# Kernel optimization log

Measured on AMD Instinct MI355X. Metric: run time of the kernel, lower is better.

## Reference

```python
import math
import jax, jax.numpy as jnp
import numpy as np

B, T, C = 4, 2048, 1024
NH = 16
HD = C // NH  # 64

def setup_inputs() -> dict:
    key = jax.random.key(0)
    k1, k2, k3 = jax.random.split(key, 3)
    x = jax.random.normal(k1, (B, T, C), dtype=jnp.float32)
    # init scale ~ 1/sqrt(fan_in) to keep activations sane
    W_attn = jax.random.normal(k2, (C, 3 * C), dtype=jnp.float32) * (1.0 / math.sqrt(C))
    b_attn = jnp.zeros((3 * C,), dtype=jnp.float32)
    W_proj = jax.random.normal(k3, (C, C), dtype=jnp.float32) * (1.0 / math.sqrt(C))
    b_proj = jnp.zeros((C,), dtype=jnp.float32)
    return {"x": x, "W_attn": W_attn, "b_attn": b_attn, "W_proj": W_proj, "b_proj": b_proj}

def reference(x, W_attn, b_attn, W_proj, b_proj):
    b, t, c = x.shape
    qkv = x @ W_attn + b_attn                      # [B,T,3C]
    q, k, v = jnp.split(qkv, 3, axis=-1)           # each [B,T,C]
    # [B,T,C] -> [B,NH,T,HD]
    def heads(z):
        return z.reshape(b, t, NH, HD).transpose(0, 2, 1, 3)
    q, k, v = heads(q), heads(k), heads(v)
    scale = 1.0 / math.sqrt(HD)
    att = jnp.einsum('bhqd,bhkd->bhqk', q, k) * scale   # [B,NH,T,T]
    causal = jnp.tril(jnp.ones((t, t), dtype=bool))      # [T,T]
    att = jnp.where(causal[None, None, :, :], att, -jnp.inf)
    att = jax.nn.softmax(att, axis=-1)
    # dropout p=0.0 -> identity
    y = jnp.einsum('bhqk,bhkd->bhqd', att, v)            # [B,NH,T,HD]
    y = y.transpose(0, 2, 1, 3).reshape(b, t, c)         # [B,T,C]
    return y @ W_proj + b_proj
```

## Files before the change

kernel.cpp:

```cpp
#include <hip/hip_runtime.h>
#include <hip/hip_bf16.h>


typedef __bf16 bf16;
typedef __bf16 bf16x4 __attribute__((ext_vector_type(4)));
typedef __bf16 bf16x8 __attribute__((ext_vector_type(8)));
typedef float  f32x4  __attribute__((ext_vector_type(4)));

#define MFMA16(a, b, c) __builtin_amdgcn_mfma_f32_16x16x32_bf16((a), (b), (c), 0, 0, 0)

#define GLOAD16(g, l)                                                 \
    __builtin_amdgcn_global_load_lds(                                 \
        (const __attribute__((address_space(1))) void*)(g),           \
        (__attribute__((address_space(3))) void*)(l), 16, 0, 0)

static constexpr int Bsz = 4;
static constexpr int T   = 2048;
static constexpr int Cc  = 1024;
static constexpr int NH  = 16;
static constexpr int HD  = 64;
static constexpr int C3  = 3 * Cc;

__global__ void cvt_f32_bf16(const float* __restrict__ in, bf16* __restrict__ out) {
    size_t i = ((size_t)blockIdx.x * blockDim.x + threadIdx.x) * 8;
    f32x4 a0 = *(const f32x4*)(in + i);
    f32x4 a1 = *(const f32x4*)(in + i + 4);
    bf16x8 v;
#pragma unroll
    for (int e = 0; e < 4; ++e) { v[e] = (bf16)a0[e]; v[e + 4] = (bf16)a1[e]; }
    *(bf16x8*)(out + i) = v;
}

__global__ void transpose_f32_bf16(const float* __restrict__ in, bf16* __restrict__ out,
                                   int R, int Ccols) {
    __shared__ float tile[32][33];
    int bx = blockIdx.x * 32;
    int by = blockIdx.y * 32;
    int tx = threadIdx.x, ty = threadIdx.y;
#pragma unroll
    for (int i = 0; i < 32; i += 8)
        tile[ty + i][tx] = in[(size_t)(by + ty + i) * Ccols + bx + tx];
    __syncthreads();
#pragma unroll
    for (int i = 0; i < 32; i += 8)
        out[(size_t)(bx + ty + i) * R + by + tx] = (bf16)tile[tx][ty + i];
}

__global__ __launch_bounds__(256)
void gemm_qkv(const bf16* __restrict__ A, const bf16* __restrict__ Bt,
              const float* __restrict__ bias,
              bf16* __restrict__ qo, bf16* __restrict__ ko, bf16* __restrict__ vt,
              int M, int N, int K) {
    constexpr int BM = 128, BN = 128, BK = 64;
    __shared__ bf16 As[2][BM * BK];
    __shared__ bf16 Bs[2][BN * BK];

    const int tid  = threadIdx.x;
    const int wave = tid >> 6, lane = tid & 63;
    const int quad = lane >> 4, l16 = lane & 15;
    const int wm = wave & 1, wn = wave >> 1;
    const int m0 = blockIdx.x * BM, n0 = blockIdx.y * BN;

    f32x4 acc[4][4] = {};

    const int lrow = lane >> 3;
    const int lcol = (lane & 7) * 8;
    const bf16* Ab = A  + (size_t)(m0 + wave * 8 + lrow) * K + lcol;
    const bf16* Bb = Bt + (size_t)(n0 + wave * 8 + lrow) * K + lcol;
    const int wofs = wave * 512;

#pragma unroll
    for (int r = 0; r < 4; ++r) {
        GLOAD16(Ab + (size_t)r * 32 * K, As[0] + wofs + r * 2048);
        GLOAD16(Bb + (size_t)r * 32 * K, Bs[0] + wofs + r * 2048);
    }

    int cur = 0;
    for (int k0 = 0; k0 < K; k0 += BK) {
        __syncthreads();
        if (k0 + BK < K) {
#pragma unroll
            for (int r = 0; r < 4; ++r) {
                GLOAD16(Ab + (size_t)r * 32 * K + k0 + BK, As[cur ^ 1] + wofs + r * 2048);
                GLOAD16(Bb + (size_t)r * 32 * K + k0 + BK, Bs[cur ^ 1] + wofs + r * 2048);
            }
        }
        const bf16* Asc = As[cur];
        const bf16* Bsc = Bs[cur];
#pragma unroll
        for (int ks = 0; ks < 2; ++ks) {
            bf16x8 af[4], bfr[4];
#pragma unroll
            for (int i = 0; i < 4; ++i)
                af[i] = *(const bf16x8*)(&Asc[(wm * 64 + i * 16 + l16) * BK + ks * 32 + quad * 8]);
#pragma unroll
            for (int j = 0; j < 4; ++j)
                bfr[j] = *(const bf16x8*)(&Bsc[(wn * 64 + j * 16 + l16) * BK + ks * 32 + quad * 8]);
#pragma unroll
            for (int i = 0; i < 4; ++i)
#pragma unroll
                for (int j = 0; j < 4; ++j)
                    acc[i][j] = MFMA16(af[i], bfr[j], acc[i][j]);
        }
        cur ^= 1;
    }

    const int which = n0 >> 10;
    const int nc0 = n0 & 1023;
    if (which < 2) {
        bf16* dst = which ? ko : qo;
#pragma unroll
        for (int j = 0; j < 4; ++j) {
            int colg = n0 + wn * 64 + j * 16 + l16;
            int coll = nc0 + wn * 64 + j * 16 + l16;
            float bv = bias[colg];
#pragma unroll
            for (int i = 0; i < 4; ++i) {
                int rowb = m0 + wm * 64 + i * 16 + quad * 4;
#pragma unroll
                for (int r = 0; r < 4; ++r)
                    dst[(size_t)(rowb + r) * Cc + coll] = (bf16)(acc[i][j][r] + bv);
            }
        }
    } else {
#pragma unroll
        for (int j = 0; j < 4; ++j) {
            int colg = n0 + wn * 64 + j * 16 + l16;
            int coll = nc0 + wn * 64 + j * 16 + l16;
            int h = coll >> 6, d = coll & 63;
            float bv = bias[colg];
            bf16* vhead_d = vt + ((size_t)h * HD + d) * T;
#pragma unroll
            for (int i = 0; i < 4; ++i) {
                int rowb = m0 + wm * 64 + i * 16 + quad * 4;
                int b = rowb >> 11;
                int t = rowb & 2047;
                bf16x4 pk;
#pragma unroll
                for (int r = 0; r < 4; ++r) pk[r] = (bf16)(acc[i][j][r] + bv);
                *(bf16x4*)(vhead_d + (size_t)b * NH * HD * T + t) = pk;
            }
        }
    }
}

__global__ __launch_bounds__(256)
void gemm_bt(const bf16* __restrict__ A, const bf16* __restrict__ Bt,
             const float* __restrict__ bias, float* __restrict__ C,
             int M, int N, int K) {
    constexpr int BM = 128, BN = 128, BK = 64;
    __shared__ bf16 As[2][BM * BK];
    __shared__ bf16 Bs[2][BN * BK];

    const int tid  = threadIdx.x;
    const int wave = tid >> 6, lane = tid & 63;
    const int quad = lane >> 4, l16 = lane & 15;
    const int wm = wave & 1, wn = wave >> 1;
    const int m0 = blockIdx.x * BM, n0 = blockIdx.y * BN;

    f32x4 acc[4][4] = {};

    const int lrow = lane >> 3;
    const int lcol = (lane & 7) * 8;
    const bf16* Ab = A  + (size_t)(m0 + wave * 8 + lrow) * K + lcol;
    const bf16* Bb = Bt + (size_t)(n0 + wave * 8 + lrow) * K + lcol;
    const int wofs = wave * 512;

#pragma unroll
    for (int r = 0; r < 4; ++r) {
        GLOAD16(Ab + (size_t)r * 32 * K, As[0] + wofs + r * 2048);
        GLOAD16(Bb + (size_t)r * 32 * K, Bs[0] + wofs + r * 2048);
    }

    int cur = 0;
    for (int k0 = 0; k0 < K; k0 += BK) {
        __syncthreads();
        if (k0 + BK < K) {
#pragma unroll
            for (int r = 0; r < 4; ++r) {
                GLOAD16(Ab + (size_t)r * 32 * K + k0 + BK, As[cur ^ 1] + wofs + r * 2048);
                GLOAD16(Bb + (size_t)r * 32 * K + k0 + BK, Bs[cur ^ 1] + wofs + r * 2048);
            }
        }
        const bf16* Asc = As[cur];
        const bf16* Bsc = Bs[cur];
#pragma unroll
        for (int ks = 0; ks < 2; ++ks) {
            bf16x8 af[4], bfr[4];
#pragma unroll
            for (int i = 0; i < 4; ++i)
                af[i] = *(const bf16x8*)(&Asc[(wm * 64 + i * 16 + l16) * BK + ks * 32 + quad * 8]);
#pragma unroll
            for (int j = 0; j < 4; ++j)
                bfr[j] = *(const bf16x8*)(&Bsc[(wn * 64 + j * 16 + l16) * BK + ks * 32 + quad * 8]);
#pragma unroll
            for (int i = 0; i < 4; ++i)
#pragma unroll
                for (int j = 0; j < 4; ++j)
                    acc[i][j] = MFMA16(af[i], bfr[j], acc[i][j]);
        }
        cur ^= 1;
    }

#pragma unroll
    for (int j = 0; j < 4; ++j) {
        int col = n0 + wn * 64 + j * 16 + l16;
        float bv = bias[col];
#pragma unroll
        for (int i = 0; i < 4; ++i) {
            int rowb = m0 + wm * 64 + i * 16 + quad * 4;
#pragma unroll
            for (int r = 0; r < 4; ++r)
                C[(size_t)(rowb + r) * N + col] = acc[i][j][r] + bv;
        }
    }
}

__global__ __launch_bounds__(256, 4)
void attn_fused(const bf16* __restrict__ qb, const bf16* __restrict__ kb,
                const bf16* __restrict__ vtb, bf16* __restrict__ y) {
    constexpr int LKD = 72;
    constexpr int LVT = 40;
    constexpr int LPS = 40;
    constexpr int QT = T / 128;
    __shared__ bf16 Ks[2][32 * LKD];
    __shared__ bf16 Vt[2][64 * LVT];
    __shared__ bf16 Ps[4][32 * LPS];

    const int tid  = threadIdx.x;
    const int wave = tid >> 6, lane = tid & 63;
    const int quad = lane >> 4, l16 = lane & 15;
    const int bid = blockIdx.x;
    const int pr = bid >> 6;
    const int hb = bid & 63;
    const int b = hb >> 4, h = hb & 15;

    const bf16* qbase  = qb + (size_t)b * T * Cc + h * HD;
    const bf16* kbase  = kb + (size_t)b * T * Cc + h * HD;
    const bf16* vthead = vtb + (size_t)(b * NH + h) * HD * T;
    bf16* yrow = y + (size_t)b * T * Cc + h * HD;

    const int srK = tid >> 3, scK = (tid & 7) * 8;
    const int srV = tid >> 2, scV = (tid & 3) * 8;

    bf16x8 ones;
#pragma unroll
    for (int e = 0; e < 8; ++e) ones[e] = (bf16)1.0f;

#pragma unroll 1
    for (int seg = 0; seg < 2; ++seg) {
        const int qt = (seg == 0) ? (QT - 1 - pr) : pr;
        const int q0 = qt * 128;

        bf16x8 qf[2][2];
#pragma unroll
        for (int qn = 0; qn < 2; ++qn) {
            int qrow = q0 + wave * 32 + qn * 16 + l16;
#pragma unroll
            for (int dblk = 0; dblk < 2; ++dblk) {
                bf16x8 v = *(const bf16x8*)(qbase + (size_t)qrow * Cc + dblk * 32 + quad * 8);
#pragma unroll
                for (int e = 0; e < 8; ++e) v[e] = (bf16)((float)v[e] * 0.18033688f);
                qf[qn][dblk] = v;
            }
        }

        f32x4 o[2][4] = {};
        f32x4 osum[2] = {};

        const int w0 = q0 + wave * 32;
        const int nt = q0 / 32 + 4;

        bf16x8 kp = *(const bf16x8*)(kbase + (size_t)srK * Cc + scK);
        bf16x8 vp = *(const bf16x8*)(vthead + (size_t)srV * T + scV);
        __syncthreads();
        *(bf16x8*)(&Ks[0][srK * LKD + scK]) = kp;
        *(bf16x8*)(&Vt[0][srV * LVT + scV]) = vp;

        int cur = 0;
        for (int it = 0; it < nt; ++it) {
            const int kt = it * 32;
            __syncthreads();

            const bool more = (it + 1 < nt);
            if (more) {
                int ktn = kt + 32;
                kp = *(const bf16x8*)(kbase + (size_t)(ktn + srK) * Cc + scK);
                vp = *(const bf16x8*)(vthead + (size_t)srV * T + ktn + scV);
            }

            const bf16* ksc = Ks[cur];
            const bf16* vtc = Vt[cur];
            if (kt <= w0 + 31) {
                __builtin_amdgcn_s_setprio(1);
                f32x4 st[2][2] = {};
#pragma unroll
                for (int km = 0; km < 2; ++km) {
                    bf16x8 kf0 = *(const bf16x8*)(&ksc[(km * 16 + l16) * LKD + quad * 8]);
                    bf16x8 kf1 = *(const bf16x8*)(&ksc[(km * 16 + l16) * LKD + 32 + quad * 8]);
#pragma unroll
                    for (int qn = 0; qn < 2; ++qn) {
                        st[km][qn] = MFMA16(kf0, qf[qn][0], st[km][qn]);
                        st[km][qn] = MFMA16(kf1, qf[qn][1], st[km][qn]);
                    }
                }

                const bool needmask = (kt + 31 > w0);
#pragma unroll
                for (int km = 0; km < 2; ++km)
#pragma unroll
                    for (int qn = 0; qn < 2; ++qn) {
                        int qrel = w0 + qn * 16 + l16 - kt;
#pragma unroll
                        for (int r = 0; r < 4; ++r) {
                            float v = st[km][qn][r];
                            if (needmask) {
                                int key = km * 16 + quad * 4 + r;
                                v = (key <= qrel) ? v : -INFINITY;
                            }
                            st[km][qn][r] = __builtin_exp2f(v);
                        }
                    }

                bf16* pw = &Ps[wave][0];
#pragma unroll
                for (int qn = 0; qn < 2; ++qn)
#pragma unroll
                    for (int km = 0; km < 2; ++km) {
                        bf16x4 pk;
#pragma unroll
                        for (int r = 0; r < 4; ++r) pk[r] = (bf16)st[km][qn][r];
                        *(bf16x4*)(&pw[(qn * 16 + l16) * LPS + km * 16 + quad * 4]) = pk;
                    }
                bf16x8 pf[2];
#pragma unroll
                for (int qn = 0; qn < 2; ++qn)
                    pf[qn] = *(const bf16x8*)(&pw[(qn * 16 + l16) * LPS + quad * 8]);

#pragma unroll
                for (int dd = 0; dd < 4; ++dd) {
                    bf16x8 vf = *(const bf16x8*)(&vtc[(dd * 16 + l16) * LVT + quad * 8]);
                    o[0][dd] = MFMA16(pf[0], vf, o[0][dd]);
                    o[1][dd] = MFMA16(pf[1], vf, o[1][dd]);
                }
                osum[0] = MFMA16(pf[0], ones, osum[0]);
                osum[1] = MFMA16(pf[1], ones, osum[1]);
                __builtin_amdgcn_s_setprio(0);
            }

            if (more) {
                *(bf16x8*)(&Ks[cur ^ 1][srK * LKD + scK]) = kp;
                *(bf16x8*)(&Vt[cur ^ 1][srV * LVT + scV]) = vp;
            }
            cur ^= 1;
        }

#pragma unroll
        for (int qn = 0; qn < 2; ++qn)
#pragma unroll
            for (int r = 0; r < 4; ++r) {
                float inv = 1.0f / osum[qn][r];
                int t = w0 + qn * 16 + quad * 4 + r;
#pragma unroll
                for (int dd = 0; dd < 4; ++dd)
                    yrow[(size_t)t * Cc + dd * 16 + l16] = (bf16)(o[qn][dd][r] * inv);
            }
    }
}

extern "C" void kernel_launch(void* const* d_in, const int* in_sizes, int n_in,
                              void* d_out, int out_size, void* d_ws, size_t ws_size,
                              hipStream_t stream) {
    const float* x      = (const float*)d_in[0];
    const float* W_attn = (const float*)d_in[1];
    const float* b_attn = (const float*)d_in[2];
    const float* W_proj = (const float*)d_in[3];
    const float* b_proj = (const float*)d_in[4];
    float* out = (float*)d_out;

    const int M = Bsz * T;
    const size_t R = (size_t)M * Cc;

    bf16* qb  = (bf16*)d_ws;
    bf16* kb  = qb + R;
    bf16* vtb = kb + R;
    bf16* xb  = vtb + R;
    bf16* yb  = xb;
    bf16* WtA = (bf16*)d_out;
    bf16* WtP = qb;

    dim3 tpb(32, 8);

    cvt_f32_bf16<<<(int)(R / (256 * 8)), 256, 0, stream>>>(x, xb);
    transpose_f32_bf16<<<dim3(C3 / 32, Cc / 32), tpb, 0, stream>>>(W_attn, WtA, Cc, C3);
    gemm_qkv<<<dim3(M / 128, C3 / 128), 256, 0, stream>>>(xb, WtA, b_attn, qb, kb, vtb, M, C3, Cc);
    attn_fused<<<512, 256, 0, stream>>>(qb, kb, vtb, yb);
    transpose_f32_bf16<<<dim3(Cc / 32, Cc / 32), tpb, 0, stream>>>(W_proj, WtP, Cc, Cc);
    gemm_bt<<<dim3(M / 128, Cc / 128), 256, 0, stream>>>(yb, WtP, b_proj, out, M, Cc, Cc);
}
```

Baseline: 285.6 us.

## Halve attention query tile to 64 rows, doubling blocks; fuse x-convert and weight transpose

The attention kernel now handles 64-query tiles, with each wave owning 16 query rows instead of 32, and launches 1024 blocks instead of 512. This gives more parallelism and finer causal load balancing across the GPU. The cost is that each K/V tile staged in shared memory is reused by half as many query rows, so K/V traffic per unit of work rises. Separately, the x bf16 conversion and the W_attn transpose are merged into one launch to save a kernel launch.

```diff
diff --git a/kernel.cpp b/kernel.cpp
--- a/kernel.cpp
+++ b/kernel.cpp
@@ -21,14 +21,32 @@
 static constexpr int HD  = 64;
 static constexpr int C3  = 3 * Cc;
 
-__global__ void cvt_f32_bf16(const float* __restrict__ in, bf16* __restrict__ out) {
-    size_t i = ((size_t)blockIdx.x * blockDim.x + threadIdx.x) * 8;
-    f32x4 a0 = *(const f32x4*)(in + i);
-    f32x4 a1 = *(const f32x4*)(in + i + 4);
-    bf16x8 v;
-#pragma unroll
-    for (int e = 0; e < 4; ++e) { v[e] = (bf16)a0[e]; v[e + 4] = (bf16)a1[e]; }
-    *(bf16x8*)(out + i) = v;
+__global__ void prep(const float* __restrict__ x, bf16* __restrict__ xb,
+                     const float* __restrict__ W_attn, bf16* __restrict__ WtA) {
+    const int bid = blockIdx.x;
+    const int tid = threadIdx.x;
+    if (bid < 4096) {
+        size_t i = ((size_t)bid * 256 + tid) * 8;
+        f32x4 a0 = *(const f32x4*)(x + i);
+        f32x4 a1 = *(const f32x4*)(x + i + 4);
+        bf16x8 v;
+#pragma unroll
+        for (int e = 0; e < 4; ++e) { v[e] = (bf16)a0[e]; v[e + 4] = (bf16)a1[e]; }
+        *(bf16x8*)(xb + i) = v;
+    } else {
+        __shared__ float tile[32][33];
+        const int tb = bid - 4096;
+        const int bx = (tb % (C3 / 32)) * 32;
+        const int by = (tb / (C3 / 32)) * 32;
+        const int tx = tid & 31, ty = tid >> 5;
+#pragma unroll
+        for (int i = 0; i < 32; i += 8)
+            tile[ty + i][tx] = W_attn[(size_t)(by + ty + i) * C3 + bx + tx];
+        __syncthreads();
+#pragma unroll
+        for (int i = 0; i < 32; i += 8)
+            WtA[(size_t)(bx + ty + i) * Cc + by + tx] = (bf16)tile[tx][ty + i];
+    }
 }
 
 __global__ void transpose_f32_bf16(const float* __restrict__ in, bf16* __restrict__ out,
@@ -222,10 +240,10 @@
     constexpr int LKD = 72;
     constexpr int LVT = 40;
     constexpr int LPS = 40;
-    constexpr int QT = T / 128;
+    constexpr int QT = T / 64;
     __shared__ bf16 Ks[2][32 * LKD];
     __shared__ bf16 Vt[2][64 * LVT];
-    __shared__ bf16 Ps[4][32 * LPS];
+    __shared__ bf16 Ps[4][16 * LPS];
 
     const int tid  = threadIdx.x;
     const int wave = tid >> 6, lane = tid & 63;
@@ -250,26 +268,25 @@
 #pragma unroll 1
     for (int seg = 0; seg < 2; ++seg) {
         const int qt = (seg == 0) ? (QT - 1 - pr) : pr;
-        const int q0 = qt * 128;
-
-        bf16x8 qf[2][2];
-#pragma unroll
-        for (int qn = 0; qn < 2; ++qn) {
-            int qrow = q0 + wave * 32 + qn * 16 + l16;
+        const int q0 = qt * 64;
+
+        bf16x8 qf[2];
+        {
+            int qrow = q0 + wave * 16 + l16;
 #pragma unroll
             for (int dblk = 0; dblk < 2; ++dblk) {
                 bf16x8 v = *(const bf16x8*)(qbase + (size_t)qrow * Cc + dblk * 32 + quad * 8);
 #pragma unroll
                 for (int e = 0; e < 8; ++e) v[e] = (bf16)((float)v[e] * 0.18033688f);
-                qf[qn][dblk] = v;
-            }
-        }
-
-        f32x4 o[2][4] = {};
-        f32x4 osum[2] = {};
-
-        const int w0 = q0 + wave * 32;
-        const int nt = q0 / 32 + 4;
+                qf[dblk] = v;
+            }
+        }
+
+        f32x4 o[4] = {};
+        f32x4 osum = {};
+
+        const int w0 = q0 + wave * 16;
+        const int nt = q0 / 32 + 2;
 
         bf16x8 kp = *(const bf16x8*)(kbase + (size_t)srK * Cc + scK);
         bf16x8 vp = *(const bf16x8*)(vthead + (size_t)srV * T + scV);
@@ -291,60 +308,47 @@
 
             const bf16* ksc = Ks[cur];
             const bf16* vtc = Vt[cur];
-            if (kt <= w0 + 31) {
+            if (kt <= w0 + 15) {
                 __builtin_amdgcn_s_setprio(1);
-                f32x4 st[2][2] = {};
+                f32x4 st[2] = {};
 #pragma unroll
                 for (int km = 0; km < 2; ++km) {
                     bf16x8 kf0 = *(const bf16x8*)(&ksc[(km * 16 + l16) * LKD + quad * 8]);
                     bf16x8 kf1 = *(const bf16x8*)(&ksc[(km * 16 + l16) * LKD + 32 + quad * 8]);
-#pragma unroll
-                    for (int qn = 0; qn < 2; ++qn) {
-                        st[km][qn] = MFMA16(kf0, qf[qn][0], st[km][qn]);
-                        st[km][qn] = MFMA16(kf1, qf[qn][1], st[km][qn]);
+                    st[km] = MFMA16(kf0, qf[0], st[km]);
+                    st[km] = MFMA16(kf1, qf[1], st[km]);
+                }
+
+                const bool needmask = (kt + 31 > w0);
+                const int qrel = w0 + l16 - kt;
+#pragma unroll
+                for (int km = 0; km < 2; ++km)
+#pragma unroll
+                    for (int r = 0; r < 4; ++r) {
+                        float v = st[km][r];
+                        if (needmask) {
+                            int key = km * 16 + quad * 4 + r;
+                            v = (key <= qrel) ? v : -INFINITY;
+                        }
+                        st[km][r] = __builtin_exp2f(v);
                     }
+
+                bf16* pw = &Ps[wave][0];
+#pragma unroll
+                for (int km = 0; km < 2; ++km) {
+                    bf16x4 pk;
+#pragma unroll
+                    for (int r = 0; r < 4; ++r) pk[r] = (bf16)st[km][r];
+                    *(bf16x4*)(&pw[l16 * LPS + km * 16 + quad * 4]) = pk;
                 }
-
-                const bool needmask = (kt + 31 > w0);
-#pragma unroll
-                for (int km = 0; km < 2; ++km)
-#pragma unroll
-                    for (int qn = 0; qn < 2; ++qn) {
-                        int qrel = w0 + qn * 16 + l16 - kt;
-#pragma unroll
-                        for (int r = 0; r < 4; ++r) {
-                            float v = st[km][qn][r];
-                            if (needmask) {
-                                int key = km * 16 + quad * 4 + r;
-                                v = (key <= qrel) ? v : -INFINITY;
-                            }
-                            st[km][qn][r] = __builtin_exp2f(v);
-                        }
-                    }
-
-                bf16* pw = &Ps[wave][0];
-#pragma unroll
-                for (int qn = 0; qn < 2; ++qn)
-#pragma unroll
-                    for (int km = 0; km < 2; ++km) {
-                        bf16x4 pk;
-#pragma unroll
-                        for (int r = 0; r < 4; ++r) pk[r] = (bf16)st[km][qn][r];
-                        *(bf16x4*)(&pw[(qn * 16 + l16) * LPS + km * 16 + quad * 4]) = pk;
-                    }
-                bf16x8 pf[2];
-#pragma unroll
-                for (int qn = 0; qn < 2; ++qn)
-                    pf[qn] = *(const bf16x8*)(&pw[(qn * 16 + l16) * LPS + quad * 8]);
+                bf16x8 pf = *(const bf16x8*)(&pw[l16 * LPS + quad * 8]);
 
 #pragma unroll
                 for (int dd = 0; dd < 4; ++dd) {
                     bf16x8 vf = *(const bf16x8*)(&vtc[(dd * 16 + l16) * LVT + quad * 8]);
-                    o[0][dd] = MFMA16(pf[0], vf, o[0][dd]);
-                    o[1][dd] = MFMA16(pf[1], vf, o[1][dd]);
+                    o[dd] = MFMA16(pf, vf, o[dd]);
                 }
-                osum[0] = MFMA16(pf[0], ones, osum[0]);
-                osum[1] = MFMA16(pf[1], ones, osum[1]);
+                osum = MFMA16(pf, ones, osum);
                 __builtin_amdgcn_s_setprio(0);
             }
 
@@ -356,15 +360,13 @@
         }
 
 #pragma unroll
-        for (int qn = 0; qn < 2; ++qn)
-#pragma unroll
-            for (int r = 0; r < 4; ++r) {
-                float inv = 1.0f / osum[qn][r];
-                int t = w0 + qn * 16 + quad * 4 + r;
-#pragma unroll
-                for (int dd = 0; dd < 4; ++dd)
-                    yrow[(size_t)t * Cc + dd * 16 + l16] = (bf16)(o[qn][dd][r] * inv);
-            }
+        for (int r = 0; r < 4; ++r) {
+            float inv = 1.0f / osum[r];
+            int t = w0 + quad * 4 + r;
+#pragma unroll
+            for (int dd = 0; dd < 4; ++dd)
+                yrow[(size_t)t * Cc + dd * 16 + l16] = (bf16)(o[dd][r] * inv);
+        }
     }
 }
 
@@ -389,12 +391,9 @@
     bf16* WtA = (bf16*)d_out;
     bf16* WtP = qb;
 
-    dim3 tpb(32, 8);
-
-    cvt_f32_bf16<<<(int)(R / (256 * 8)), 256, 0, stream>>>(x, xb);
-    transpose_f32_bf16<<<dim3(C3 / 32, Cc / 32), tpb, 0, stream>>>(W_attn, WtA, Cc, C3);
+    prep<<<4096 + 3072, 256, 0, stream>>>(x, xb, W_attn, WtA);
     gemm_qkv<<<dim3(M / 128, C3 / 128), 256, 0, stream>>>(xb, WtA, b_attn, qb, kb, vtb, M, C3, Cc);
-    attn_fused<<<512, 256, 0, stream>>>(qb, kb, vtb, yb);
-    transpose_f32_bf16<<<dim3(Cc / 32, Cc / 32), tpb, 0, stream>>>(W_proj, WtP, Cc, Cc);
+    attn_fused<<<1024, 256, 0, stream>>>(qb, kb, vtb, yb);
+    transpose_f32_bf16<<<dim3(Cc / 32, Cc / 32), dim3(32, 8), 0, stream>>>(W_proj, WtP, Cc, Cc);
     gemm_bt<<<dim3(M / 128, Cc / 128), 256, 0, stream>>>(yb, WtP, b_proj, out, M, Cc, Cc);
 }
```

Result: faster. 274.4 us (-3.9%).
